# Kernel tuning notes

Measured on AMD Instinct MI355X. Metric: run time of the kernel, lower is better.

## Reference

```python
import jax, jax.numpy as jnp
import numpy as np

N = 100000   # nodes
M = 50000    # hyperedges
E = 600000   # incidences
D_IN = 128
D_OUT = 128


def setup_inputs() -> dict:
    key = jax.random.key(0)
    ks = jax.random.split(key, 7)
    x = jax.random.normal(ks[0], (N, D_IN), dtype=jnp.float32)
    row = jax.random.randint(ks[1], (E,), 0, N, dtype=jnp.int64)  # node ids
    col = jax.random.randint(ks[2], (E,), 0, M, dtype=jnp.int64)  # hyperedge ids
    edge_index = jnp.stack([row, col], axis=0)
    s_v = 1.0 / np.sqrt(D_IN)
    s_e = 1.0 / np.sqrt(D_OUT)
    s_u = 1.0 / np.sqrt(2 * D_OUT)
    W_v = jax.random.uniform(ks[3], (D_IN, D_OUT), jnp.float32, -s_v, s_v)
    W_e = jax.random.uniform(ks[4], (D_OUT, D_OUT), jnp.float32, -s_e, s_e)
    W_upd = jax.random.uniform(ks[5], (2 * D_OUT, D_OUT), jnp.float32, -s_u, s_u)
    b_upd = jax.random.uniform(ks[6], (D_OUT,), jnp.float32, -s_u, s_u)
    return {"x": x, "edge_index": edge_index, "W_v": W_v, "W_e": W_e,
            "W_upd": W_upd, "b_upd": b_upd}


def _mean_reduce(vals, index, K):
    # vals: (E, D); scatter-mean into (K, D)
    s = jax.ops.segment_sum(vals, index, num_segments=K)
    cnt = jax.ops.segment_sum(jnp.ones((vals.shape[0], 1), vals.dtype), index,
                              num_segments=K)
    return s / jnp.maximum(cnt, 1.0)


def reference(x, edge_index, W_v, W_e, W_upd, b_upd):
    row, col = edge_index[0], edge_index[1]
    x_self = x @ W_v                                # (N, D)
    # vertex -> hyperedge (mean pooling)
    e_feat = _mean_reduce(x_self[row], col, M)      # (M, D)
    e_proj = e_feat @ W_e                           # (M, D)
    # hyperedge -> vertex (mean pooling)
    n_agg = _mean_reduce(e_proj[col], row, N)       # (N, D)
    out = jnp.concatenate([x_self, n_agg], axis=-1) # (N, 2D)
    return jax.nn.relu(out @ W_upd + b_upd)
```

## Files before the change

### kernel.cpp

```cpp
#include <hip/hip_runtime.h>

typedef unsigned short u16;
typedef unsigned int u32;
typedef __attribute__((ext_vector_type(8))) short bf16x8;
typedef __attribute__((ext_vector_type(4))) float f32x4;

__device__ inline u16 f2bf(float f) {
    u32 u = __float_as_uint(f);
    return (u16)((u + 0x7FFFu + ((u >> 16) & 1u)) >> 16);
}
__device__ inline bf16x8 pack8(float4 a, float4 b) {
    bf16x8 v = { (short)f2bf(a.x), (short)f2bf(a.y), (short)f2bf(a.z), (short)f2bf(a.w),
                 (short)f2bf(b.x), (short)f2bf(b.y), (short)f2bf(b.z), (short)f2bf(b.w) };
    return v;
}
__device__ inline float bflo(u32 v) { return __uint_as_float(v << 16); }
__device__ inline float bfhi(u32 v) { return __uint_as_float(v & 0xFFFF0000u); }

#define LDA 136
#define CAPE 64
#define CAPN 48
#define PE   6250
#define PN   12500

__device__ inline void gemm128_nolds(
    const float* __restrict__ A, const float* __restrict__ B, int tile,
    u16* __restrict__ Wt, int koff, float* __restrict__ Cf32)
{
    const int tid = threadIdx.x;
    const int col = tid & 127;
    const int rh  = tid >> 7;
    const int r0  = tile * 16;
    float acc[8] = {0.f,0.f,0.f,0.f,0.f,0.f,0.f,0.f};
    for (int k = 0; k < 128; ++k) {
        float bv = B[(size_t)k * 128 + col];
        #pragma unroll
        for (int i = 0; i < 8; ++i)
            acc[i] = fmaf(A[(size_t)(r0 + rh * 8 + i) * 128 + k], bv, acc[i]);
    }
    #pragma unroll
    for (int i = 0; i < 8; ++i) {
        int r = r0 + rh * 8 + i;
        if (Wt)   Wt[(size_t)col * 256 + koff + r] = f2bf(acc[i]);
        if (Cf32) Cf32[(size_t)r * 128 + col] = acc[i];
    }
}

__global__ __launch_bounds__(256) void fill_conv(
    const int* __restrict__ row, const int* __restrict__ col,
    int* __restrict__ cnt_e, int* __restrict__ cnt_n,
    int* __restrict__ adj_e, u16* __restrict__ adj_n, int E, int nbFill8,
    const float* __restrict__ x, u16* __restrict__ xb, size_t n8,
    const float* __restrict__ W_v, const float* __restrict__ W_e,
    const float* __restrict__ W_upd, float* __restrict__ T,
    u16* __restrict__ Wt)
{
    u32 bid = blockIdx.x;
    if (bid < 16) {
        if (bid < 8) gemm128_nolds(W_v, W_upd, bid, Wt, 0, nullptr);
        else         gemm128_nolds(W_e, W_upd + 128 * 128, bid - 8, nullptr, 0, T);
        return;
    }
    bid -= 16;
    if (bid < (u32)nbFill8) {
        const int chunk = bid >> 3;
        const int part  = bid & 7;
        const int e = chunk * 256 + threadIdx.x;
        if (e >= E) return;
        const int r = row[e], c = col[e];
        if ((u32)c / PE == (u32)part) {
            int pe = atomicAdd(&cnt_e[c], 1);
            if (pe < CAPE) adj_e[(size_t)c * CAPE + pe] = r;
        }
        if ((u32)r / PN == (u32)part) {
            int pn = atomicAdd(&cnt_n[r], 1);
            if (pn < CAPN) adj_n[(size_t)r * CAPN + pn] = (u16)c;
        }
        return;
    }
    bid -= nbFill8;
    size_t i = (size_t)bid * 256 + threadIdx.x;
    if (i < n8) {
        const float4* s = (const float4*)(x + i * 8);
        *(bf16x8*)(xb + i * 8) = pack8(s[0], s[1]);
    }
}

__device__ inline int4 load4idx(const int* a, int k) {
    uint4 v = *(const uint4*)(a + k);
    return make_int4((int)v.x, (int)v.y, (int)v.z, (int)v.w);
}
__device__ inline int4 load4idx(const u16* a, int k) {
    ushort4 v = *(const ushort4*)(a + k);
    return make_int4(v.x, v.y, v.z, v.w);
}

template<typename IDX, int CAP>
__device__ inline void gather4_body(
    const u32* __restrict__ src, const IDX* __restrict__ adj,
    const int* __restrict__ cnt, u32* __restrict__ out, int K, int rowBase)
{
    const int tid = threadIdx.x;
    const int row = rowBase + (tid >> 4);
    const int l16 = tid & 15;
    if (row >= K) return;
    int d = cnt[row];
    if (d > CAP) d = CAP;
    const IDX* a = adj + (size_t)row * CAP;
    float a0=0,a1=0,a2=0,a3=0,a4=0,a5=0,a6=0,a7=0;
    float b0=0,b1=0,b2=0,b3=0,b4=0,b5=0,b6=0,b7=0;
    int k = 0;
    for (; k + 4 <= d; k += 4) {
        int4 idx = load4idx(a, k);
        uint4 v0 = *(const uint4*)(src + (size_t)(u32)idx.x * 64 + l16 * 4);
        uint4 v1 = *(const uint4*)(src + (size_t)(u32)idx.y * 64 + l16 * 4);
        uint4 v2 = *(const uint4*)(src + (size_t)(u32)idx.z * 64 + l16 * 4);
        uint4 v3 = *(const uint4*)(src + (size_t)(u32)idx.w * 64 + l16 * 4);
        a0+=bflo(v0.x); a1+=bfhi(v0.x); a2+=bflo(v0.y); a3+=bfhi(v0.y);
        a4+=bflo(v0.z); a5+=bfhi(v0.z); a6+=bflo(v0.w); a7+=bfhi(v0.w);
        b0+=bflo(v1.x); b1+=bfhi(v1.x); b2+=bflo(v1.y); b3+=bfhi(v1.y);
        b4+=bflo(v1.z); b5+=bfhi(v1.z); b6+=bflo(v1.w); b7+=bfhi(v1.w);
        a0+=bflo(v2.x); a1+=bfhi(v2.x); a2+=bflo(v2.y); a3+=bfhi(v2.y);
        a4+=bflo(v2.z); a5+=bfhi(v2.z); a6+=bflo(v2.w); a7+=bfhi(v2.w);
        b0+=bflo(v3.x); b1+=bfhi(v3.x); b2+=bflo(v3.y); b3+=bfhi(v3.y);
        b4+=bflo(v3.z); b5+=bfhi(v3.z); b6+=bflo(v3.w); b7+=bfhi(v3.w);
    }
    for (; k < d; ++k) {
        uint4 v = *(const uint4*)(src + (size_t)(u32)a[k] * 64 + l16 * 4);
        a0+=bflo(v.x); a1+=bfhi(v.x); a2+=bflo(v.y); a3+=bfhi(v.y);
        a4+=bflo(v.z); a5+=bfhi(v.z); a6+=bflo(v.w); a7+=bfhi(v.w);
    }
    float inv = 1.f / fmaxf((float)d, 1.f);
    float s0=(a0+b0)*inv, s1=(a1+b1)*inv, s2=(a2+b2)*inv, s3=(a3+b3)*inv;
    float s4=(a4+b4)*inv, s5=(a5+b5)*inv, s6=(a6+b6)*inv, s7=(a7+b7)*inv;
    uint4 res;
    res.x = ((u32)f2bf(s1) << 16) | (u32)f2bf(s0);
    res.y = ((u32)f2bf(s3) << 16) | (u32)f2bf(s2);
    res.z = ((u32)f2bf(s5) << 16) | (u32)f2bf(s4);
    res.w = ((u32)f2bf(s7) << 16) | (u32)f2bf(s6);
    *(uint4*)(out + (size_t)row * 64 + l16 * 4) = res;
}

__global__ __launch_bounds__(256) void gather_e_k(
    const u32* __restrict__ src, const int* __restrict__ adj,
    const int* __restrict__ cnt, u32* __restrict__ out, int K,
    const float* __restrict__ W_v, const float* __restrict__ T,
    u16* __restrict__ Wt)
{
    if (blockIdx.x < 8) {
        gemm128_nolds(W_v, T, blockIdx.x, Wt, 128, nullptr);
        return;
    }
    gather4_body<int, CAPE>(src, adj, cnt, out, K, (blockIdx.x - 8) * 16);
}

__global__ __launch_bounds__(256) void gather_n_k(
    const u32* __restrict__ src, const u16* __restrict__ adj,
    const int* __restrict__ cnt, u32* __restrict__ out, int K)
{
    gather4_body<u16, CAPN>(src, adj, cnt, out, K, blockIdx.x * 16);
}

__global__ __launch_bounds__(256) void mfma_gemm_final(
    const u16* __restrict__ Xbf, const u16* __restrict__ Nbf,
    const u16* __restrict__ Wt, const float* __restrict__ bias,
    float* __restrict__ C, int nrows)
{
    __shared__ u16 Bsh[128 * LDA];
    const int tid = threadIdx.x;
    const int r0 = blockIdx.x * 64;
    const int w = tid >> 6, lane = tid & 63;
    const int lr = lane & 15, lk = (lane >> 4) << 3;
    const int arow = r0 + w * 16 + lr;

    f32x4 acc[8] = { {0,0,0,0},{0,0,0,0},{0,0,0,0},{0,0,0,0},
                     {0,0,0,0},{0,0,0,0},{0,0,0,0},{0,0,0,0} };

    for (int ph = 0; ph < 2; ++ph) {
        __syncthreads();
        const u16* Asrc = ph ? Nbf : Xbf;
        #pragma unroll
        for (int p = 0; p < 8; ++p) {
            int chunk = p * 256 + tid;
            int n = chunk >> 4, kg = (chunk & 15) << 3;
            *(bf16x8*)&Bsh[n * LDA + kg] =
                *(const bf16x8*)(Wt + (size_t)n * 256 + ph * 128 + kg);
        }
        __syncthreads();
        #pragma unroll
        for (int ks = 0; ks < 4; ++ks) {
            bf16x8 af = {0,0,0,0,0,0,0,0};
            if (arow < nrows)
                af = *(const bf16x8*)(Asrc + (size_t)arow * 128 + ks * 32 + lk);
            #pragma unroll
            for (int t = 0; t < 8; ++t) {
                bf16x8 bfr = *(bf16x8*)&Bsh[(t * 16 + lr) * LDA + ks * 32 + lk];
                acc[t] = __builtin_amdgcn_mfma_f32_16x16x32_bf16(af, bfr, acc[t], 0, 0, 0);
            }
        }
    }

    const int rbase = r0 + w * 16 + ((lane >> 4) << 2);
    #pragma unroll
    for (int t = 0; t < 8; ++t) {
        int gc = t * 16 + lr;
        float bv = bias[gc];
        #pragma unroll
        for (int reg = 0; reg < 4; ++reg) {
            int gr = rbase + reg;
            if (gr < nrows)
                __builtin_nontemporal_store(fmaxf(acc[t][reg] + bv, 0.f),
                                            C + (size_t)gr * 128 + gc);
        }
    }
}

extern "C" void kernel_launch(void* const* d_in, const int* in_sizes, int n_in,
                              void* d_out, int out_size, void* d_ws, size_t ws_size,
                              hipStream_t stream)
{
    const float* x     = (const float*)d_in[0];
    const int*   ei    = (const int*)  d_in[1];
    const float* W_v   = (const float*)d_in[2];
    const float* W_e   = (const float*)d_in[3];
    const float* W_upd = (const float*)d_in[4];
    const float* b_upd = (const float*)d_in[5];

    const int N = in_sizes[0] / 128;
    const int E = in_sizes[1] / 2;
    const int M = 50000;

    const int* row = ei;
    const int* col = ei + E;

    char* p = (char*)d_ws;
    u16* x_bf   = (u16*)p;  p += (size_t)N * 128 * 2;
    u16* xbar   = (u16*)p;  p += (size_t)M * 128 * 2;
    u16* nbar   = (u16*)p;  p += (size_t)N * 128 * 2;
    float* T    = (float*)p; p += 128 * 128 * 4;
    u16* Wt     = (u16*)p;  p += 128 * 256 * 2;
    int* cnt_e  = (int*)p;  p += (size_t)M * 4;
    int* cnt_n  = (int*)p;  p += (size_t)N * 4;
    int* adj_e  = (int*)p;  p += (size_t)M * CAPE * 4;
    u16* adj_n  = (u16*)p;  p += (size_t)N * CAPN * 2;

    const int nchunks = (E + 255) / 256;
    const int nbFill8 = nchunks * 8;
    const size_t n8 = (size_t)N * 128 / 8;
    const int nbConv = (int)((n8 + 255) / 256);

    hipMemsetAsync(cnt_e, 0, (size_t)(M + N) * sizeof(int), stream);

    fill_conv<<<16 + nbFill8 + nbConv, 256, 0, stream>>>(
        row, col, cnt_e, cnt_n, adj_e, adj_n, E, nbFill8,
        x, x_bf, n8, W_v, W_e, W_upd, T, Wt);

    gather_e_k<<<8 + (M + 15) / 16, 256, 0, stream>>>(
        (const u32*)x_bf, adj_e, cnt_e, (u32*)xbar, M, W_v, T, Wt);

    gather_n_k<<<(N + 15) / 16, 256, 0, stream>>>(
        (const u32*)xbar, adj_n, cnt_n, (u32*)nbar, N);

    mfma_gemm_final<<<(N + 63) / 64, 256, 0, stream>>>(
        x_bf, nbar, Wt, b_upd, (float*)d_out, N);
}
```

Before: 151.5 us.

## Move node-adjacency fill into the hyperedge gather kernel to overlap work

The node-side CSR fill (atomic counts into cnt_n and writes to adj_n) moves out of the first kernel and into the second, where it runs as extra blocks next to the hyperedge gather. This shortens the first kernel and lets the node atomics overlap with the memory-bound gather instead of contending with the hyperedge atomics. The cost is a second read of row/col and extra blocks in the gather launch, with fill blocks scheduled ahead of gather blocks.

```diff
diff --git a/kernel.cpp b/kernel.cpp
--- a/kernel.cpp
+++ b/kernel.cpp
@@ -46,10 +46,9 @@
     }
 }
 
-__global__ __launch_bounds__(256) void fill_conv(
+__global__ __launch_bounds__(256) void k1_fill_e(
     const int* __restrict__ row, const int* __restrict__ col,
-    int* __restrict__ cnt_e, int* __restrict__ cnt_n,
-    int* __restrict__ adj_e, u16* __restrict__ adj_n, int E, int nbFill8,
+    int* __restrict__ cnt_e, int* __restrict__ adj_e, int E, int nbFill8,
     const float* __restrict__ x, u16* __restrict__ xb, size_t n8,
     const float* __restrict__ W_v, const float* __restrict__ W_e,
     const float* __restrict__ W_upd, float* __restrict__ T,
@@ -67,14 +66,10 @@
         const int part  = bid & 7;
         const int e = chunk * 256 + threadIdx.x;
         if (e >= E) return;
-        const int r = row[e], c = col[e];
+        const int c = col[e];
         if ((u32)c / PE == (u32)part) {
             int pe = atomicAdd(&cnt_e[c], 1);
-            if (pe < CAPE) adj_e[(size_t)c * CAPE + pe] = r;
-        }
-        if ((u32)r / PN == (u32)part) {
-            int pn = atomicAdd(&cnt_n[r], 1);
-            if (pn < CAPN) adj_n[(size_t)r * CAPN + pn] = (u16)c;
+            if (pe < CAPE) adj_e[(size_t)c * CAPE + pe] = row[e];
         }
         return;
     }
@@ -141,17 +136,34 @@
     *(uint4*)(out + (size_t)row * 64 + l16 * 4) = res;
 }
 
-__global__ __launch_bounds__(256) void gather_e_k(
-    const u32* __restrict__ src, const int* __restrict__ adj,
-    const int* __restrict__ cnt, u32* __restrict__ out, int K,
+__global__ __launch_bounds__(256) void k2_gather_e_fill_n(
+    const int* __restrict__ row, const int* __restrict__ col,
+    int* __restrict__ cnt_n, u16* __restrict__ adj_n, int E, int nbFill8,
+    const u32* __restrict__ src, const int* __restrict__ adj_e,
+    const int* __restrict__ cnt_e, u32* __restrict__ out, int K,
     const float* __restrict__ W_v, const float* __restrict__ T,
     u16* __restrict__ Wt)
 {
-    if (blockIdx.x < 8) {
-        gemm128_nolds(W_v, T, blockIdx.x, Wt, 128, nullptr);
-        return;
-    }
-    gather4_body<int, CAPE>(src, adj, cnt, out, K, (blockIdx.x - 8) * 16);
+    u32 bid = blockIdx.x;
+    if (bid < 8) {
+        gemm128_nolds(W_v, T, bid, Wt, 128, nullptr);
+        return;
+    }
+    bid -= 8;
+    if (bid < (u32)nbFill8) {
+        const int chunk = bid >> 3;
+        const int part  = bid & 7;
+        const int e = chunk * 256 + threadIdx.x;
+        if (e >= E) return;
+        const int r = row[e];
+        if ((u32)r / PN == (u32)part) {
+            int pn = atomicAdd(&cnt_n[r], 1);
+            if (pn < CAPN) adj_n[(size_t)r * CAPN + pn] = (u16)col[e];
+        }
+        return;
+    }
+    bid -= nbFill8;
+    gather4_body<int, CAPE>(src, adj_e, cnt_e, out, K, bid * 16);
 }
 
 __global__ __launch_bounds__(256) void gather_n_k(
@@ -251,11 +263,12 @@
 
     hipMemsetAsync(cnt_e, 0, (size_t)(M + N) * sizeof(int), stream);
 
-    fill_conv<<<16 + nbFill8 + nbConv, 256, 0, stream>>>(
-        row, col, cnt_e, cnt_n, adj_e, adj_n, E, nbFill8,
+    k1_fill_e<<<16 + nbFill8 + nbConv, 256, 0, stream>>>(
+        row, col, cnt_e, adj_e, E, nbFill8,
         x, x_bf, n8, W_v, W_e, W_upd, T, Wt);
 
-    gather_e_k<<<8 + (M + 15) / 16, 256, 0, stream>>>(
+    k2_gather_e_fill_n<<<8 + nbFill8 + (M + 15) / 16, 256, 0, stream>>>(
+        row, col, cnt_n, adj_n, E, nbFill8,
         (const u32*)x_bf, adj_e, cnt_e, (u32*)xbar, M, W_v, T, Wt);
 
     gather_n_k<<<(N + 15) / 16, 256, 0, stream>>>(
```

After: 155.4 us. 1.03x slower.
